# Performance work log

Hardware: AMD Instinct MI355X
Metric: run time of the kernel (lower is better)

Reference implementation:

```python
import jax, jax.numpy as jnp
import numpy as np

EPS = 0.1  # global `eps` in original repo (width scale)


def _parts(x, c, w):
    # x: (N,3), c: (N1,3), w: (N1,3)
    x1 = x[:, 0:1] - c[:, 0]  # (N, N1)
    y1 = x[:, 1:2] - c[:, 1]
    z1 = x[:, 2:3] - c[:, 2]
    d = w * w  # (N1, 3)
    e = jnp.exp(-(x1 * x1 * d[:, 0] + y1 * y1 * d[:, 1] + z1 * z1 * d[:, 2]))
    return x1, y1, z1, d, e


def _u(e, h):
    return e @ h  # (N,)


def _du(diff, dcoef, e, h):
    return ((-2.0 * diff * dcoef) * e) @ h  # (N,)


def setup_inputs() -> dict:
    key = jax.random.key(0)
    ks = jax.random.split(key, 13)
    N, N1 = 32768, 1024
    x = jax.random.uniform(ks[0], (N, 3), dtype=jnp.float32)
    def params(k1, k2, k3):
        h = jax.random.uniform(k1, (N1,), dtype=jnp.float32)
        c = jax.random.uniform(k2, (N1, 3), dtype=jnp.float32)
        w = 5.0 * jax.random.uniform(k3, (N1, 3), dtype=jnp.float32) / EPS
        return h, c, w
    h1, c1, w1 = params(ks[1], ks[2], ks[3])
    h2, c2, w2 = params(ks[4], ks[5], ks[6])
    h3, c3, w3 = params(ks[7], ks[8], ks[9])
    h4, c4, w4 = params(ks[10], ks[11], ks[12])
    return {"x": x, "h1": h1, "c1": c1, "w1": w1,
            "h2": h2, "c2": c2, "w2": w2,
            "h3": h3, "c3": c3, "w3": w3,
            "h4": h4, "c4": c4, "w4": w4}


def reference(x, h1, c1, w1, h2, c2, w2, h3, c3, w3, h4, c4, w4):
    # Set 1: ux, uy, uz (kernel exp computed once, reused for all 3 derivs)
    x1, y1, z1, d, e = _parts(x, c1, w1)
    ux = _du(x1, d[:, 0], e, h1)
    uy = _du(y1, d[:, 1], e, h1)
    uz = _du(z1, d[:, 2], e, h1)
    # Set 2: P, Px
    x1, y1, z1, d, e = _parts(x, c2, w2)
    P = _u(e, h2)
    Px = _du(x1, d[:, 0], e, h2)
    # Set 3: Q, Qy
    x1, y1, z1, d, e = _parts(x, c3, w3)
    Q = _u(e, h3)
    Qy = _du(y1, d[:, 1], e, h3)
    # Set 4: R, Rz
    x1, y1, z1, d, e = _parts(x, c4, w4)
    R = _u(e, h4)
    Rz = _du(z1, d[:, 2], e, h4)
    return (ux, uy, uz, P, Px, Q, Qy, R, Rz)
```

## Files before the change

kernel.cpp:

```cpp
#include <hip/hip_runtime.h>

typedef float v2f __attribute__((ext_vector_type(2)));

static constexpr float SQRT_LOG2E = 1.2011224087864498f;
static constexpr float NEG_2LN2   = -1.3862943611198906f;

__device__ __forceinline__ v2f sp(float s) { return (v2f){s, s}; }
__device__ __forceinline__ v2f vfma(v2f a, v2f b, v2f c) {
    return __builtin_elementwise_fma(a, b, c);
}

template <int SET>
__device__ __forceinline__ void srbf_body(
    const float* __restrict__ x, const float* __restrict__ h,
    const float* __restrict__ c, const float* __restrict__ w,
    float* __restrict__ dst, int N, int jbase, int jcount, float4* lds)
{
    constexpr int REC = (SET == 0) ? 3 : 2;
    constexpr int OB  = (SET == 0) ? 0 : (2 * SET + 1);
    const int tid = threadIdx.x;

    for (int jj = tid; jj < jcount; jj += 256) {
        const int gj = jbase + jj;
        float hj  = h[gj];
        float w0  = w[3 * gj + 0] * SQRT_LOG2E;
        float w1  = w[3 * gj + 1] * SQRT_LOG2E;
        float w2  = w[3 * gj + 2] * SQRT_LOG2E;
        float cw0 = -c[3 * gj + 0] * w0;
        float cw1 = -c[3 * gj + 1] * w1;
        float cw2 = -c[3 * gj + 2] * w2;
        if constexpr (SET == 0) {
            lds[jj * 3 + 0] = make_float4(w0, w1, w2, cw0);
            lds[jj * 3 + 1] = make_float4(cw1, cw2, NEG_2LN2 * hj * w0, NEG_2LN2 * hj * w1);
            lds[jj * 3 + 2] = make_float4(NEG_2LN2 * hj * w2, 0.f, 0.f, 0.f);
        } else {
            constexpr int K = SET - 1;
            float wk = (K == 0) ? w0 : (K == 1 ? w1 : w2);
            lds[jj * 2 + 0] = make_float4(w0, w1, w2, cw0);
            lds[jj * 2 + 1] = make_float4(cw1, cw2, hj, NEG_2LN2 * hj * wk);
        }
    }
    __syncthreads();

    const int i0 = blockIdx.x * 1024 + tid;
    v2f px[2], py[2], pz[2];
#pragma unroll
    for (int g = 0; g < 2; ++g) {
        const int ia = i0 + 512 * g, ib = ia + 256;
        px[g] = (v2f){x[3 * ia + 0], x[3 * ib + 0]};
        py[g] = (v2f){x[3 * ia + 1], x[3 * ib + 1]};
        pz[g] = (v2f){x[3 * ia + 2], x[3 * ib + 2]};
    }

    v2f a0[2] = {sp(0.f), sp(0.f)};
    v2f a1[2] = {sp(0.f), sp(0.f)};
    v2f a2[2] = {sp(0.f), sp(0.f)};

#pragma unroll 4
    for (int jj = 0; jj < jcount; ++jj) {
        const float4 A = lds[jj * REC + 0];
        const float4 B = lds[jj * REC + 1];
        float b2c = 0.f;
        if constexpr (SET == 0) b2c = lds[jj * 3 + 2].x;
#pragma unroll
        for (int g = 0; g < 2; ++g) {
            v2f t0 = vfma(px[g], sp(A.x), sp(A.w));
            v2f t1 = vfma(py[g], sp(A.y), sp(B.x));
            v2f t2 = vfma(pz[g], sp(A.z), sp(B.y));
            v2f s  = vfma(t0, t0, vfma(t1, t1, t2 * t2));
            v2f e  = (v2f){__builtin_amdgcn_exp2f(-s.x),
                           __builtin_amdgcn_exp2f(-s.y)};
            if constexpr (SET == 0) {
                a0[g] = vfma(t0, sp(B.z) * e, a0[g]);
                a1[g] = vfma(t1, sp(B.w) * e, a1[g]);
                a2[g] = vfma(t2, sp(b2c) * e, a2[g]);
            } else {
                constexpr int K = SET - 1;
                v2f tk = (K == 0) ? t0 : (K == 1 ? t1 : t2);
                a0[g] = vfma(sp(B.z), e, a0[g]);
                a1[g] = vfma(tk, sp(B.w) * e, a1[g]);
            }
        }
    }

#pragma unroll
    for (int g = 0; g < 2; ++g) {
        const int ia = i0 + 512 * g, ib = ia + 256;
        dst[(OB + 0) * N + ia] = a0[g].x;  dst[(OB + 0) * N + ib] = a0[g].y;
        dst[(OB + 1) * N + ia] = a1[g].x;  dst[(OB + 1) * N + ib] = a1[g].y;
        if constexpr (SET == 0) {
            dst[2 * N + ia] = a2[g].x;     dst[2 * N + ib] = a2[g].y;
        }
    }
}

__global__ __launch_bounds__(256) void srbf_kernel(
    const float* x,
    const float* h1, const float* c1, const float* w1,
    const float* h2, const float* c2, const float* w2,
    const float* h3, const float* c3, const float* w3,
    const float* h4, const float* c4, const float* w4,
    float* out, float* ws, int N, int jcount, int split)
{
    extern __shared__ float4 lds[];
    const int jbase = blockIdx.y * jcount;
    float* dst = (split > 1) ? (ws + (size_t)blockIdx.y * 9 * N) : out;
    switch (blockIdx.z) {
    case 0: srbf_body<0>(x, h1, c1, w1, dst, N, jbase, jcount, lds); break;
    case 1: srbf_body<1>(x, h2, c2, w2, dst, N, jbase, jcount, lds); break;
    case 2: srbf_body<2>(x, h3, c3, w3, dst, N, jbase, jcount, lds); break;
    case 3: srbf_body<3>(x, h4, c4, w4, dst, N, jbase, jcount, lds); break;
    }
}

__global__ __launch_bounds__(256) void reduce_kernel(
    const float4* __restrict__ ws, float4* __restrict__ out,
    int total4, int split)
{
    const int i = blockIdx.x * 256 + threadIdx.x;
    if (i < total4) {
        float4 acc = ws[i];
#pragma unroll 8
        for (int p = 1; p < split; ++p) {
            const float4 v = ws[(size_t)p * total4 + i];
            acc.x += v.x; acc.y += v.y; acc.z += v.z; acc.w += v.w;
        }
        out[i] = acc;
    }
}

extern "C" void kernel_launch(void* const* d_in, const int* in_sizes, int n_in,
                              void* d_out, int out_size, void* d_ws, size_t ws_size,
                              hipStream_t stream)
{
    const float* x = (const float*)d_in[0];
    const int N  = in_sizes[0] / 3;
    const int N1 = in_sizes[1];

    int split = 1;
    for (int s = 8; s >= 2; s >>= 1) {
        if (ws_size >= (size_t)s * 9 * N * sizeof(float) && (N1 % s) == 0) {
            split = s; break;
        }
    }
    const int jcount = N1 / split;

    dim3 grid(N / 1024, split, 4);
    const size_t lds_bytes = (size_t)jcount * 3 * sizeof(float4);
    srbf_kernel<<<grid, 256, lds_bytes, stream>>>(
        x,
        (const float*)d_in[1],  (const float*)d_in[2],  (const float*)d_in[3],
        (const float*)d_in[4],  (const float*)d_in[5],  (const float*)d_in[6],
        (const float*)d_in[7],  (const float*)d_in[8],  (const float*)d_in[9],
        (const float*)d_in[10], (const float*)d_in[11], (const float*)d_in[12],
        (float*)d_out, (float*)d_ws, N, jcount, split);

    if (split > 1) {
        const int total4 = 9 * N / 4;
        reduce_kernel<<<(total4 + 255) / 256, 256, 0, stream>>>(
            (const float4*)d_ws, (float4*)d_out, total4, split);
    }
}
```

Measured before the change: 39.17 us.

## Use single-wave blocks with scalar math, 4 points per thread, and split up to 16

```diff
diff --git a/kernel.cpp b/kernel.cpp
--- a/kernel.cpp
+++ b/kernel.cpp
@@ -1,26 +1,19 @@
 #include <hip/hip_runtime.h>
-
-typedef float v2f __attribute__((ext_vector_type(2)));
 
 static constexpr float SQRT_LOG2E = 1.2011224087864498f;
 static constexpr float NEG_2LN2   = -1.3862943611198906f;
-
-__device__ __forceinline__ v2f sp(float s) { return (v2f){s, s}; }
-__device__ __forceinline__ v2f vfma(v2f a, v2f b, v2f c) {
-    return __builtin_elementwise_fma(a, b, c);
-}
 
 template <int SET>
 __device__ __forceinline__ void srbf_body(
     const float* __restrict__ x, const float* __restrict__ h,
     const float* __restrict__ c, const float* __restrict__ w,
-    float* __restrict__ dst, int N, int jbase, int jcount, float4* lds)
+    float* __restrict__ dst, int N, int jbase, int jcount, float4* lds4)
 {
-    constexpr int REC = (SET == 0) ? 3 : 2;
-    constexpr int OB  = (SET == 0) ? 0 : (2 * SET + 1);
+    constexpr int OB = (SET == 0) ? 0 : (2 * SET + 1);
     const int tid = threadIdx.x;
+    float* ldsb2 = (float*)(lds4 + 2 * jcount);
 
-    for (int jj = tid; jj < jcount; jj += 256) {
+    for (int jj = tid; jj < jcount; jj += 64) {
         const int gj = jbase + jj;
         float hj  = h[gj];
         float w0  = w[3 * gj + 0] * SQRT_LOG2E;
@@ -29,72 +22,66 @@
         float cw0 = -c[3 * gj + 0] * w0;
         float cw1 = -c[3 * gj + 1] * w1;
         float cw2 = -c[3 * gj + 2] * w2;
+        lds4[jj * 2 + 0] = make_float4(w0, w1, w2, cw0);
         if constexpr (SET == 0) {
-            lds[jj * 3 + 0] = make_float4(w0, w1, w2, cw0);
-            lds[jj * 3 + 1] = make_float4(cw1, cw2, NEG_2LN2 * hj * w0, NEG_2LN2 * hj * w1);
-            lds[jj * 3 + 2] = make_float4(NEG_2LN2 * hj * w2, 0.f, 0.f, 0.f);
+            lds4[jj * 2 + 1] = make_float4(cw1, cw2, NEG_2LN2 * hj * w0,
+                                           NEG_2LN2 * hj * w1);
+            ldsb2[jj] = NEG_2LN2 * hj * w2;
         } else {
             constexpr int K = SET - 1;
             float wk = (K == 0) ? w0 : (K == 1 ? w1 : w2);
-            lds[jj * 2 + 0] = make_float4(w0, w1, w2, cw0);
-            lds[jj * 2 + 1] = make_float4(cw1, cw2, hj, NEG_2LN2 * hj * wk);
+            lds4[jj * 2 + 1] = make_float4(cw1, cw2, hj, NEG_2LN2 * hj * wk);
         }
     }
     __syncthreads();
 
-    const int i0 = blockIdx.x * 1024 + tid;
-    v2f px[2], py[2], pz[2];
+    const int i0 = blockIdx.x * 256 + tid;
+    float px[4], py[4], pz[4], a0[4], a1[4], a2[4];
 #pragma unroll
-    for (int g = 0; g < 2; ++g) {
-        const int ia = i0 + 512 * g, ib = ia + 256;
-        px[g] = (v2f){x[3 * ia + 0], x[3 * ib + 0]};
-        py[g] = (v2f){x[3 * ia + 1], x[3 * ib + 1]};
-        pz[g] = (v2f){x[3 * ia + 2], x[3 * ib + 2]};
+    for (int g = 0; g < 4; ++g) {
+        const int ia = i0 + 64 * g;
+        px[g] = x[3 * ia + 0];
+        py[g] = x[3 * ia + 1];
+        pz[g] = x[3 * ia + 2];
+        a0[g] = a1[g] = a2[g] = 0.f;
     }
-
-    v2f a0[2] = {sp(0.f), sp(0.f)};
-    v2f a1[2] = {sp(0.f), sp(0.f)};
-    v2f a2[2] = {sp(0.f), sp(0.f)};
 
 #pragma unroll 4
     for (int jj = 0; jj < jcount; ++jj) {
-        const float4 A = lds[jj * REC + 0];
-        const float4 B = lds[jj * REC + 1];
-        float b2c = 0.f;
-        if constexpr (SET == 0) b2c = lds[jj * 3 + 2].x;
+        const float4 A = lds4[jj * 2 + 0];
+        const float4 B = lds4[jj * 2 + 1];
+        float b2 = 0.f;
+        if constexpr (SET == 0) b2 = ldsb2[jj];
 #pragma unroll
-        for (int g = 0; g < 2; ++g) {
-            v2f t0 = vfma(px[g], sp(A.x), sp(A.w));
-            v2f t1 = vfma(py[g], sp(A.y), sp(B.x));
-            v2f t2 = vfma(pz[g], sp(A.z), sp(B.y));
-            v2f s  = vfma(t0, t0, vfma(t1, t1, t2 * t2));
-            v2f e  = (v2f){__builtin_amdgcn_exp2f(-s.x),
-                           __builtin_amdgcn_exp2f(-s.y)};
+        for (int g = 0; g < 4; ++g) {
+            float t0 = fmaf(px[g], A.x, A.w);
+            float t1 = fmaf(py[g], A.y, B.x);
+            float t2 = fmaf(pz[g], A.z, B.y);
+            float s  = fmaf(t0, t0, fmaf(t1, t1, t2 * t2));
+            float e  = __builtin_amdgcn_exp2f(-s);
             if constexpr (SET == 0) {
-                a0[g] = vfma(t0, sp(B.z) * e, a0[g]);
-                a1[g] = vfma(t1, sp(B.w) * e, a1[g]);
-                a2[g] = vfma(t2, sp(b2c) * e, a2[g]);
+                a0[g] = fmaf(t0, B.z * e, a0[g]);
+                a1[g] = fmaf(t1, B.w * e, a1[g]);
+                a2[g] = fmaf(t2, b2 * e, a2[g]);
             } else {
                 constexpr int K = SET - 1;
-                v2f tk = (K == 0) ? t0 : (K == 1 ? t1 : t2);
-                a0[g] = vfma(sp(B.z), e, a0[g]);
-                a1[g] = vfma(tk, sp(B.w) * e, a1[g]);
+                float tk = (K == 0) ? t0 : (K == 1 ? t1 : t2);
+                a0[g] = fmaf(B.z, e, a0[g]);
+                a1[g] = fmaf(tk, B.w * e, a1[g]);
             }
         }
     }
 
 #pragma unroll
-    for (int g = 0; g < 2; ++g) {
-        const int ia = i0 + 512 * g, ib = ia + 256;
-        dst[(OB + 0) * N + ia] = a0[g].x;  dst[(OB + 0) * N + ib] = a0[g].y;
-        dst[(OB + 1) * N + ia] = a1[g].x;  dst[(OB + 1) * N + ib] = a1[g].y;
-        if constexpr (SET == 0) {
-            dst[2 * N + ia] = a2[g].x;     dst[2 * N + ib] = a2[g].y;
-        }
+    for (int g = 0; g < 4; ++g) {
+        const int ia = i0 + 64 * g;
+        dst[(OB + 0) * N + ia] = a0[g];
+        dst[(OB + 1) * N + ia] = a1[g];
+        if constexpr (SET == 0) dst[2 * N + ia] = a2[g];
     }
 }
 
-__global__ __launch_bounds__(256) void srbf_kernel(
+__global__ __launch_bounds__(64, 8) void srbf_kernel(
     const float* x,
     const float* h1, const float* c1, const float* w1,
     const float* h2, const float* c2, const float* w2,
@@ -102,14 +89,14 @@
     const float* h4, const float* c4, const float* w4,
     float* out, float* ws, int N, int jcount, int split)
 {
-    extern __shared__ float4 lds[];
+    extern __shared__ float4 lds4[];
     const int jbase = blockIdx.y * jcount;
     float* dst = (split > 1) ? (ws + (size_t)blockIdx.y * 9 * N) : out;
     switch (blockIdx.z) {
-    case 0: srbf_body<0>(x, h1, c1, w1, dst, N, jbase, jcount, lds); break;
-    case 1: srbf_body<1>(x, h2, c2, w2, dst, N, jbase, jcount, lds); break;
-    case 2: srbf_body<2>(x, h3, c3, w3, dst, N, jbase, jcount, lds); break;
-    case 3: srbf_body<3>(x, h4, c4, w4, dst, N, jbase, jcount, lds); break;
+    case 0: srbf_body<0>(x, h1, c1, w1, dst, N, jbase, jcount, lds4); break;
+    case 1: srbf_body<1>(x, h2, c2, w2, dst, N, jbase, jcount, lds4); break;
+    case 2: srbf_body<2>(x, h3, c3, w3, dst, N, jbase, jcount, lds4); break;
+    case 3: srbf_body<3>(x, h4, c4, w4, dst, N, jbase, jcount, lds4); break;
     }
 }
 
@@ -120,7 +107,7 @@
     const int i = blockIdx.x * 256 + threadIdx.x;
     if (i < total4) {
         float4 acc = ws[i];
-#pragma unroll 8
+#pragma unroll 16
         for (int p = 1; p < split; ++p) {
             const float4 v = ws[(size_t)p * total4 + i];
             acc.x += v.x; acc.y += v.y; acc.z += v.z; acc.w += v.w;
@@ -138,16 +125,16 @@
     const int N1 = in_sizes[1];
 
     int split = 1;
-    for (int s = 8; s >= 2; s >>= 1) {
+    for (int s = 16; s >= 2; s >>= 1) {
         if (ws_size >= (size_t)s * 9 * N * sizeof(float) && (N1 % s) == 0) {
             split = s; break;
         }
     }
     const int jcount = N1 / split;
 
-    dim3 grid(N / 1024, split, 4);
-    const size_t lds_bytes = (size_t)jcount * 3 * sizeof(float4);
-    srbf_kernel<<<grid, 256, lds_bytes, stream>>>(
+    dim3 grid(N / 256, split, 4);
+    const size_t lds_bytes = (size_t)jcount * (2 * sizeof(float4) + sizeof(float));
+    srbf_kernel<<<grid, 64, lds_bytes, stream>>>(
         x,
         (const float*)d_in[1],  (const float*)d_in[2],  (const float*)d_in[3],
         (const float*)d_in[4],  (const float*)d_in[5],  (const float*)d_in[6],
```

Measured after the change: 50.50 us. 28.9% more time.

## Compact LDS record for set 0, raise split-K to 16, add occupancy bound

Applied to the files above, without the earlier changes.

```diff
diff --git a/kernel.cpp b/kernel.cpp
--- a/kernel.cpp
+++ b/kernel.cpp
@@ -14,11 +14,11 @@
 __device__ __forceinline__ void srbf_body(
     const float* __restrict__ x, const float* __restrict__ h,
     const float* __restrict__ c, const float* __restrict__ w,
-    float* __restrict__ dst, int N, int jbase, int jcount, float4* lds)
+    float* __restrict__ dst, int N, int jbase, int jcount, float4* lds4)
 {
-    constexpr int REC = (SET == 0) ? 3 : 2;
-    constexpr int OB  = (SET == 0) ? 0 : (2 * SET + 1);
+    constexpr int OB = (SET == 0) ? 0 : (2 * SET + 1);
     const int tid = threadIdx.x;
+    float* ldsb2 = (float*)(lds4 + 2 * jcount);
 
     for (int jj = tid; jj < jcount; jj += 256) {
         const int gj = jbase + jj;
@@ -29,15 +29,15 @@
         float cw0 = -c[3 * gj + 0] * w0;
         float cw1 = -c[3 * gj + 1] * w1;
         float cw2 = -c[3 * gj + 2] * w2;
+        lds4[jj * 2 + 0] = make_float4(w0, w1, w2, cw0);
         if constexpr (SET == 0) {
-            lds[jj * 3 + 0] = make_float4(w0, w1, w2, cw0);
-            lds[jj * 3 + 1] = make_float4(cw1, cw2, NEG_2LN2 * hj * w0, NEG_2LN2 * hj * w1);
-            lds[jj * 3 + 2] = make_float4(NEG_2LN2 * hj * w2, 0.f, 0.f, 0.f);
+            lds4[jj * 2 + 1] = make_float4(cw1, cw2, NEG_2LN2 * hj * w0,
+                                           NEG_2LN2 * hj * w1);
+            ldsb2[jj] = NEG_2LN2 * hj * w2;
         } else {
             constexpr int K = SET - 1;
             float wk = (K == 0) ? w0 : (K == 1 ? w1 : w2);
-            lds[jj * 2 + 0] = make_float4(w0, w1, w2, cw0);
-            lds[jj * 2 + 1] = make_float4(cw1, cw2, hj, NEG_2LN2 * hj * wk);
+            lds4[jj * 2 + 1] = make_float4(cw1, cw2, hj, NEG_2LN2 * hj * wk);
         }
     }
     __syncthreads();
@@ -56,12 +56,12 @@
     v2f a1[2] = {sp(0.f), sp(0.f)};
     v2f a2[2] = {sp(0.f), sp(0.f)};
 
-#pragma unroll 4
+#pragma unroll 2
     for (int jj = 0; jj < jcount; ++jj) {
-        const float4 A = lds[jj * REC + 0];
-        const float4 B = lds[jj * REC + 1];
-        float b2c = 0.f;
-        if constexpr (SET == 0) b2c = lds[jj * 3 + 2].x;
+        const float4 A = lds4[jj * 2 + 0];
+        const float4 B = lds4[jj * 2 + 1];
+        float b2 = 0.f;
+        if constexpr (SET == 0) b2 = ldsb2[jj];
 #pragma unroll
         for (int g = 0; g < 2; ++g) {
             v2f t0 = vfma(px[g], sp(A.x), sp(A.w));
@@ -73,7 +73,7 @@
             if constexpr (SET == 0) {
                 a0[g] = vfma(t0, sp(B.z) * e, a0[g]);
                 a1[g] = vfma(t1, sp(B.w) * e, a1[g]);
-                a2[g] = vfma(t2, sp(b2c) * e, a2[g]);
+                a2[g] = vfma(t2, sp(b2)  * e, a2[g]);
             } else {
                 constexpr int K = SET - 1;
                 v2f tk = (K == 0) ? t0 : (K == 1 ? t1 : t2);
@@ -94,7 +94,7 @@
     }
 }
 
-__global__ __launch_bounds__(256) void srbf_kernel(
+__global__ __launch_bounds__(256, 8) void srbf_kernel(
     const float* x,
     const float* h1, const float* c1, const float* w1,
     const float* h2, const float* c2, const float* w2,
@@ -102,14 +102,14 @@
     const float* h4, const float* c4, const float* w4,
     float* out, float* ws, int N, int jcount, int split)
 {
-    extern __shared__ float4 lds[];
+    extern __shared__ float4 lds4[];
     const int jbase = blockIdx.y * jcount;
     float* dst = (split > 1) ? (ws + (size_t)blockIdx.y * 9 * N) : out;
     switch (blockIdx.z) {
-    case 0: srbf_body<0>(x, h1, c1, w1, dst, N, jbase, jcount, lds); break;
-    case 1: srbf_body<1>(x, h2, c2, w2, dst, N, jbase, jcount, lds); break;
-    case 2: srbf_body<2>(x, h3, c3, w3, dst, N, jbase, jcount, lds); break;
-    case 3: srbf_body<3>(x, h4, c4, w4, dst, N, jbase, jcount, lds); break;
+    case 0: srbf_body<0>(x, h1, c1, w1, dst, N, jbase, jcount, lds4); break;
+    case 1: srbf_body<1>(x, h2, c2, w2, dst, N, jbase, jcount, lds4); break;
+    case 2: srbf_body<2>(x, h3, c3, w3, dst, N, jbase, jcount, lds4); break;
+    case 3: srbf_body<3>(x, h4, c4, w4, dst, N, jbase, jcount, lds4); break;
     }
 }
 
@@ -120,7 +120,7 @@
     const int i = blockIdx.x * 256 + threadIdx.x;
     if (i < total4) {
         float4 acc = ws[i];
-#pragma unroll 8
+#pragma unroll 16
         for (int p = 1; p < split; ++p) {
             const float4 v = ws[(size_t)p * total4 + i];
             acc.x += v.x; acc.y += v.y; acc.z += v.z; acc.w += v.w;
@@ -138,7 +138,7 @@
     const int N1 = in_sizes[1];
 
     int split = 1;
-    for (int s = 8; s >= 2; s >>= 1) {
+    for (int s = 16; s >= 2; s >>= 1) {
         if (ws_size >= (size_t)s * 9 * N * sizeof(float) && (N1 % s) == 0) {
             split = s; break;
         }
@@ -146,7 +146,7 @@
     const int jcount = N1 / split;
 
     dim3 grid(N / 1024, split, 4);
-    const size_t lds_bytes = (size_t)jcount * 3 * sizeof(float4);
+    const size_t lds_bytes = (size_t)jcount * (2 * sizeof(float4) + sizeof(float));
     srbf_kernel<<<grid, 256, lds_bytes, stream>>>(
         x,
         (const float*)d_in[1],  (const float*)d_in[2],  (const float*)d_in[3],
```

Measured after the change: 40.31 us. 1.03x slower.
